# Kernel optimization log

Measured on AMD Instinct MI355X. Metric: run time of the kernel, lower is better.

The kernel has to match this reference:

```python
import jax, jax.numpy as jnp
import numpy as np

B, H, W, C = 16, 256, 256, 32
FILTER = 64


def conv_relu(x, k, b):
    y = jax.lax.conv_general_dilated(x, k, (1, 1), 'VALID',
                                     dimension_numbers=('NHWC', 'HWIO', 'NHWC'))
    return jax.nn.relu(y + b)


def maxpool2(x):
    return jax.lax.reduce_window(x, -jnp.inf, jax.lax.max,
                                 (1, 2, 2, 1), (1, 2, 2, 1), 'VALID')


def affine_grid_generator(theta):
    # tf.meshgrid default 'xy': shapes [W, H]
    xs = jnp.linspace(-1.0, 1.0, H)
    ys = jnp.linspace(-1.0, 1.0, W)
    xT, yT = jnp.meshgrid(xs, ys)
    grid = jnp.stack([xT.ravel(), yT.ravel(), jnp.ones(W * H, jnp.float32)])  # [3, W*H]
    batch_grid = jnp.einsum('bij,jk->bik', theta, grid)  # [B,2,W*H]
    return batch_grid.reshape(B, 2, H, W)


def get_pixel_value(fm, xi, yi):
    b = jnp.arange(B)[:, None, None]
    return fm[b, yi, xi]  # [B,H,W,C]


def bilinear_sampler(fm, x, y):
    max_x = H - 1
    max_y = W - 1
    x = 0.5 * ((x + 1.0) * jnp.float32(max_x - 1))
    y = 0.5 * ((y + 1.0) * jnp.float32(max_y - 1))
    x0 = jnp.floor(x).astype(jnp.int32)
    x1 = x0 + 1
    y0 = jnp.floor(y).astype(jnp.int32)
    y1 = y0 + 1
    x0 = jnp.clip(x0, 0, max_x)
    x1 = jnp.clip(x1, 0, max_x)
    y0 = jnp.clip(y0, 0, max_y)
    y1 = jnp.clip(y1, 0, max_y)
    Ia = get_pixel_value(fm, x0, y0)
    Ib = get_pixel_value(fm, x0, y1)
    Ic = get_pixel_value(fm, x1, y0)
    Id = get_pixel_value(fm, x1, y1)
    x0f, x1f = x0.astype(jnp.float32), x1.astype(jnp.float32)
    y0f, y1f = y0.astype(jnp.float32), y1.astype(jnp.float32)
    wa = ((x1f - x) * (y1f - y))[..., None]
    wb = ((x1f - x) * (y - y0f))[..., None]
    wc = ((x - x0f) * (y1f - y))[..., None]
    wd = ((x - x0f) * (y - y0f))[..., None]
    return wa * Ia + wb * Ib + wc * Ic + wd * Id


def setup_inputs() -> dict:
    key = jax.random.key(0)
    ks = jax.random.split(key, 12)

    def he(k, shape, fan_in):
        return jax.random.normal(k, shape, jnp.float32) * np.sqrt(2.0 / fan_in)

    f4, f2 = FILTER // 4, FILTER // 2
    x = jax.random.normal(ks[0], (B, H, W, C), jnp.float32)
    W1 = he(ks[1], (3, 3, C, f4), 9 * C); b1 = jnp.zeros((f4,), jnp.float32)
    W2 = he(ks[2], (3, 3, f4, f2), 9 * f4); b2 = jnp.zeros((f2,), jnp.float32)
    W3 = he(ks[3], (3, 3, f2, f2), 9 * f2); b3 = jnp.zeros((f2,), jnp.float32)
    D1 = he(ks[4], (f2, FILTER), f2); db1 = jnp.zeros((FILTER,), jnp.float32)
    D2 = he(ks[5], (FILTER, f2), FILTER); db2 = jnp.zeros((f2,), jnp.float32)
    # original inits kernel to zeros, bias to identity transform; use small
    # random kernel so the sampled grid is a non-trivial near-identity warp.
    D3 = jax.random.normal(ks[6], (f2, 6), jnp.float32) * 0.01
    db3 = jnp.array([1.0, 0.0, 0.0, 0.0, 1.0, 0.0], jnp.float32)
    return {"x": x, "W1": W1, "b1": b1, "W2": W2, "b2": b2, "W3": W3, "b3": b3,
            "D1": D1, "db1": db1, "D2": D2, "db2": db2, "D3": D3, "db3": db3}


def reference(x, W1, b1, W2, b2, W3, b3, D1, db1, D2, db2, D3, db3):
    # localization net
    h = maxpool2(conv_relu(x, W1, b1))
    h = maxpool2(conv_relu(h, W2, b2))
    h = maxpool2(conv_relu(h, W3, b3))
    h = jnp.mean(h, axis=(1, 2))  # GlobalAveragePooling2D -> [B, filter//2]
    h = jax.nn.relu(h @ D1 + db1)
    h = jax.nn.relu(h @ D2 + db2)
    theta = (h @ D3 + db3).reshape(B, 2, 3)
    grid = affine_grid_generator(theta)
    xS = grid[:, 0]
    yS = grid[:, 1]
    return bilinear_sampler(x, xS, yS)
```

## Files before the change

### kernel.cpp

```cpp
#include <hip/hip_runtime.h>
#include <hip/hip_bf16.h>


#define P1_ELEMS 4129024
#define P2_ELEMS 1968128
#define P3_ELEMS 460800

#define C1_PXSTR 36
#define C1_ROWSTR (34*36)

__global__ __launch_bounds__(256) void conv1_pool_kernel(
    const float* __restrict__ x, const float* __restrict__ W1,
    const float* __restrict__ b1, float* __restrict__ p1)
{
    __shared__ float xt[10 * C1_ROWSTR];

    const int tid = threadIdx.x;
    const int b   = blockIdx.z;
    const int ph0 = blockIdx.y * 4;
    const int pw0 = blockIdx.x * 16;
    const float* xb = x + (size_t)b * (256*256*32);

    for (int i = tid; i < 10*34*8; i += 256) {
        const int dr  = i / 272;
        const int rem = i - dr * 272;
        const int j   = rem >> 3;
        const int ch  = rem & 7;
        int r_in = 2*ph0 + dr; if (r_in > 255) r_in = 255;
        int c_in = 2*pw0 + j;  if (c_in > 255) c_in = 255;
        const float4 v = *(const float4*)(xb + ((size_t)r_in*256 + c_in)*32 + ch*4);
        *(float4*)(&xt[dr*C1_ROWSTR + j*C1_PXSTR + ch*4]) = v;
    }
    __syncthreads();

    const int fq   = __builtin_amdgcn_readfirstlane(tid >> 6);
    const int lane = tid & 63;
    const int row  = lane >> 4;
    const int col  = lane & 15;

    float4 a0, a1, a2, a3;
    {
        const float4 bv = *(const float4*)(b1 + 4*fq);
        a0 = bv; a1 = bv; a2 = bv; a3 = bv;
    }

    const float* xbase = &xt[(2*row)*C1_ROWSTR + (2*col)*C1_PXSTR];
    const float* wbase = W1 + 4*fq;

#define C1_FMA(A, XV) \
    A.x += XV.x*w0.x; A.y += XV.x*w0.y; A.z += XV.x*w0.z; A.w += XV.x*w0.w; \
    A.x += XV.y*w1.x; A.y += XV.y*w1.y; A.z += XV.y*w1.z; A.w += XV.y*w1.w; \
    A.x += XV.z*w2.x; A.y += XV.z*w2.y; A.z += XV.z*w2.z; A.w += XV.z*w2.w; \
    A.x += XV.w*w3.x; A.y += XV.w*w3.y; A.z += XV.w*w3.z; A.w += XV.w*w3.w;

    #pragma unroll 1
    for (int kh = 0; kh < 3; ++kh) {
      #pragma unroll 1
      for (int kw = 0; kw < 3; ++kw) {
        const float* xp_ = xbase + kh*C1_ROWSTR + kw*C1_PXSTR;
        const float* wp_ = wbase + (kh*3 + kw)*32*16;
        #pragma unroll
        for (int c4 = 0; c4 < 8; ++c4) {
            const float4 x0 = *(const float4*)(xp_ + 4*c4);
            const float4 x1 = *(const float4*)(xp_ + C1_PXSTR + 4*c4);
            const float4 x2 = *(const float4*)(xp_ + C1_ROWSTR + 4*c4);
            const float4 x3 = *(const float4*)(xp_ + C1_ROWSTR + C1_PXSTR + 4*c4);
            const float4 w0 = *(const float4*)(wp_ + (4*c4+0)*16);
            const float4 w1 = *(const float4*)(wp_ + (4*c4+1)*16);
            const float4 w2 = *(const float4*)(wp_ + (4*c4+2)*16);
            const float4 w3 = *(const float4*)(wp_ + (4*c4+3)*16);
            C1_FMA(a0, x0)
            C1_FMA(a1, x1)
            C1_FMA(a2, x2)
            C1_FMA(a3, x3)
        }
      }
    }

    const int ph = ph0 + row, pw = pw0 + col;
    if (ph < 127 && pw < 127) {
        float4 o;
        o.x = fmaxf(fmaxf(fmaxf(a0.x, a1.x), fmaxf(a2.x, a3.x)), 0.0f);
        o.y = fmaxf(fmaxf(fmaxf(a0.y, a1.y), fmaxf(a2.y, a3.y)), 0.0f);
        o.z = fmaxf(fmaxf(fmaxf(a0.z, a1.z), fmaxf(a2.z, a3.z)), 0.0f);
        o.w = fmaxf(fmaxf(fmaxf(a0.w, a1.w), fmaxf(a2.w, a3.w)), 0.0f);
        *(float4*)(p1 + (((size_t)b*127 + ph)*127 + pw) * 16 + 4*fq) = o;
    }
}

#define C2_PXSTR 20
#define C2_ROWSTR (34*20)

__global__ __launch_bounds__(256) void conv2_pool_kernel(
    const float* __restrict__ p1, const float* __restrict__ W2,
    const float* __restrict__ b2, float* __restrict__ p2)
{
    __shared__ float xt[10 * C2_ROWSTR];

    const int tid = threadIdx.x;
    const int b   = blockIdx.z;
    const int ph0 = blockIdx.y * 4;
    const int pw0 = blockIdx.x * 16;
    const float* xb = p1 + (size_t)b * (127*127*16);

    for (int i = tid; i < 10*34*4; i += 256) {
        const int dr  = i / 136;
        const int rem = i - dr * 136;
        const int j   = rem >> 2;
        const int ch  = rem & 3;
        int r_in = 2*ph0 + dr; if (r_in > 126) r_in = 126;
        int c_in = 2*pw0 + j;  if (c_in > 126) c_in = 126;
        const float4 v = *(const float4*)(xb + ((size_t)r_in*127 + c_in)*16 + ch*4);
        *(float4*)(&xt[dr*C2_ROWSTR + j*C2_PXSTR + ch*4]) = v;
    }
    __syncthreads();

    const int wv   = __builtin_amdgcn_readfirstlane(tid >> 6);
    const int lane = tid & 63;
    const int row  = lane >> 4;
    const int col  = lane & 15;
    const int f0   = 8 * wv;

    float4 aA0, aA1, aA2, aA3;
    float4 aB0, aB1, aB2, aB3;
    {
        const float4 bvA = *(const float4*)(b2 + f0);
        const float4 bvB = *(const float4*)(b2 + f0 + 4);
        aA0 = bvA; aA1 = bvA; aA2 = bvA; aA3 = bvA;
        aB0 = bvB; aB1 = bvB; aB2 = bvB; aB3 = bvB;
    }

    const float* xbase = &xt[(2*row)*C2_ROWSTR + (2*col)*C2_PXSTR];
    const float* wbase = W2 + f0;

#define C2_FMA(AA, AB, XC, WA, WB) \
    AA.x += XC*WA.x; AA.y += XC*WA.y; AA.z += XC*WA.z; AA.w += XC*WA.w; \
    AB.x += XC*WB.x; AB.y += XC*WB.y; AB.z += XC*WB.z; AB.w += XC*WB.w;

    #pragma unroll 1
    for (int kh = 0; kh < 3; ++kh) {
      #pragma unroll 1
      for (int kw = 0; kw < 3; ++kw) {
        const float* xp_ = xbase + kh*C2_ROWSTR + kw*C2_PXSTR;
        const float* wp_ = wbase + (kh*3 + kw)*16*32;
        #pragma unroll
        for (int c4 = 0; c4 < 4; ++c4) {
            const float4 x0 = *(const float4*)(xp_ + 4*c4);
            const float4 x1 = *(const float4*)(xp_ + C2_PXSTR + 4*c4);
            const float4 x2 = *(const float4*)(xp_ + C2_ROWSTR + 4*c4);
            const float4 x3 = *(const float4*)(xp_ + C2_ROWSTR + C2_PXSTR + 4*c4);
            #pragma unroll
            for (int c = 0; c < 4; ++c) {
                const float4 wA = *(const float4*)(wp_ + (4*c4+c)*32);
                const float4 wB = *(const float4*)(wp_ + (4*c4+c)*32 + 4);
                const float xc0 = (c==0)?x0.x:(c==1)?x0.y:(c==2)?x0.z:x0.w;
                const float xc1 = (c==0)?x1.x:(c==1)?x1.y:(c==2)?x1.z:x1.w;
                const float xc2 = (c==0)?x2.x:(c==1)?x2.y:(c==2)?x2.z:x2.w;
                const float xc3 = (c==0)?x3.x:(c==1)?x3.y:(c==2)?x3.z:x3.w;
                C2_FMA(aA0, aB0, xc0, wA, wB)
                C2_FMA(aA1, aB1, xc1, wA, wB)
                C2_FMA(aA2, aB2, xc2, wA, wB)
                C2_FMA(aA3, aB3, xc3, wA, wB)
            }
        }
      }
    }

    const int ph = ph0 + row, pw = pw0 + col;
    if (ph < 62 && pw < 62) {
        float4 oA, oB;
        oA.x = fmaxf(fmaxf(fmaxf(aA0.x, aA1.x), fmaxf(aA2.x, aA3.x)), 0.0f);
        oA.y = fmaxf(fmaxf(fmaxf(aA0.y, aA1.y), fmaxf(aA2.y, aA3.y)), 0.0f);
        oA.z = fmaxf(fmaxf(fmaxf(aA0.z, aA1.z), fmaxf(aA2.z, aA3.z)), 0.0f);
        oA.w = fmaxf(fmaxf(fmaxf(aA0.w, aA1.w), fmaxf(aA2.w, aA3.w)), 0.0f);
        oB.x = fmaxf(fmaxf(fmaxf(aB0.x, aB1.x), fmaxf(aB2.x, aB3.x)), 0.0f);
        oB.y = fmaxf(fmaxf(fmaxf(aB0.y, aB1.y), fmaxf(aB2.y, aB3.y)), 0.0f);
        oB.z = fmaxf(fmaxf(fmaxf(aB0.z, aB1.z), fmaxf(aB2.z, aB3.z)), 0.0f);
        oB.w = fmaxf(fmaxf(fmaxf(aB0.w, aB1.w), fmaxf(aB2.w, aB3.w)), 0.0f);
        float* dst = p2 + (((size_t)b*62 + ph)*62 + pw) * 32 + f0;
        *(float4*)(dst)     = oA;
        *(float4*)(dst + 4) = oB;
    }
}

__global__ __launch_bounds__(256) void conv3_pool_kernel(
    const float* __restrict__ p2, const float* __restrict__ W3,
    const float* __restrict__ b3, float* __restrict__ p3)
{
    __shared__ float xt[10 * C1_ROWSTR];

    const int tid = threadIdx.x;
    const int b   = blockIdx.z;
    const int ph0 = blockIdx.y * 4;
    const int pw0 = blockIdx.x * 16;
    const float* xb = p2 + (size_t)b * (62*62*32);

    for (int i = tid; i < 10*34*8; i += 256) {
        const int dr  = i / 272;
        const int rem = i - dr * 272;
        const int j   = rem >> 3;
        const int ch  = rem & 7;
        int r_in = 2*ph0 + dr; if (r_in > 61) r_in = 61;
        int c_in = 2*pw0 + j;  if (c_in > 61) c_in = 61;
        const float4 v = *(const float4*)(xb + ((size_t)r_in*62 + c_in)*32 + ch*4);
        *(float4*)(&xt[dr*C1_ROWSTR + j*C1_PXSTR + ch*4]) = v;
    }
    __syncthreads();

    const int wv   = __builtin_amdgcn_readfirstlane(tid >> 6);
    const int lane = tid & 63;
    const int row  = lane >> 4;
    const int col  = lane & 15;
    const int f0   = 8 * wv;

    float4 aA0, aA1, aA2, aA3;
    float4 aB0, aB1, aB2, aB3;
    {
        const float4 bvA = *(const float4*)(b3 + f0);
        const float4 bvB = *(const float4*)(b3 + f0 + 4);
        aA0 = bvA; aA1 = bvA; aA2 = bvA; aA3 = bvA;
        aB0 = bvB; aB1 = bvB; aB2 = bvB; aB3 = bvB;
    }

    const float* xbase = &xt[(2*row)*C1_ROWSTR + (2*col)*C1_PXSTR];
    const float* wbase = W3 + f0;

    #pragma unroll 1
    for (int kh = 0; kh < 3; ++kh) {
      #pragma unroll 1
      for (int kw = 0; kw < 3; ++kw) {
        const float* xp_ = xbase + kh*C1_ROWSTR + kw*C1_PXSTR;
        const float* wp_ = wbase + (kh*3 + kw)*32*32;
        #pragma unroll
        for (int c4 = 0; c4 < 8; ++c4) {
            const float4 x0 = *(const float4*)(xp_ + 4*c4);
            const float4 x1 = *(const float4*)(xp_ + C1_PXSTR + 4*c4);
            const float4 x2 = *(const float4*)(xp_ + C1_ROWSTR + 4*c4);
            const float4 x3 = *(const float4*)(xp_ + C1_ROWSTR + C1_PXSTR + 4*c4);
            #pragma unroll
            for (int c = 0; c < 4; ++c) {
                const float4 wA = *(const float4*)(wp_ + (4*c4+c)*32);
                const float4 wB = *(const float4*)(wp_ + (4*c4+c)*32 + 4);
                const float xc0 = (c==0)?x0.x:(c==1)?x0.y:(c==2)?x0.z:x0.w;
                const float xc1 = (c==0)?x1.x:(c==1)?x1.y:(c==2)?x1.z:x1.w;
                const float xc2 = (c==0)?x2.x:(c==1)?x2.y:(c==2)?x2.z:x2.w;
                const float xc3 = (c==0)?x3.x:(c==1)?x3.y:(c==2)?x3.z:x3.w;
                C2_FMA(aA0, aB0, xc0, wA, wB)
                C2_FMA(aA1, aB1, xc1, wA, wB)
                C2_FMA(aA2, aB2, xc2, wA, wB)
                C2_FMA(aA3, aB3, xc3, wA, wB)
            }
        }
      }
    }

    const int ph = ph0 + row, pw = pw0 + col;
    if (ph < 30 && pw < 30) {
        float4 oA, oB;
        oA.x = fmaxf(fmaxf(fmaxf(aA0.x, aA1.x), fmaxf(aA2.x, aA3.x)), 0.0f);
        oA.y = fmaxf(fmaxf(fmaxf(aA0.y, aA1.y), fmaxf(aA2.y, aA3.y)), 0.0f);
        oA.z = fmaxf(fmaxf(fmaxf(aA0.z, aA1.z), fmaxf(aA2.z, aA3.z)), 0.0f);
        oA.w = fmaxf(fmaxf(fmaxf(aA0.w, aA1.w), fmaxf(aA2.w, aA3.w)), 0.0f);
        oB.x = fmaxf(fmaxf(fmaxf(aB0.x, aB1.x), fmaxf(aB2.x, aB3.x)), 0.0f);
        oB.y = fmaxf(fmaxf(fmaxf(aB0.y, aB1.y), fmaxf(aB2.y, aB3.y)), 0.0f);
        oB.z = fmaxf(fmaxf(fmaxf(aB0.z, aB1.z), fmaxf(aB2.z, aB3.z)), 0.0f);
        oB.w = fmaxf(fmaxf(fmaxf(aB0.w, aB1.w), fmaxf(aB2.w, aB3.w)), 0.0f);
        float* dst = p3 + (((size_t)b*30 + ph)*30 + pw) * 32 + f0;
        *(float4*)(dst)     = oA;
        *(float4*)(dst + 4) = oB;
    }
}

__global__ __launch_bounds__(256) void head_kernel(
    const float* __restrict__ p3,
    const float* __restrict__ D1, const float* __restrict__ db1,
    const float* __restrict__ D2, const float* __restrict__ db2,
    const float* __restrict__ D3, const float* __restrict__ db3,
    float* __restrict__ theta)
{
    __shared__ float red[8][32];
    __shared__ float hmean[32];
    __shared__ float h1[64];
    __shared__ float h2[32];

    const int b   = blockIdx.x;
    const int tid = threadIdx.x;
    const int c = tid & 31, r = tid >> 5;

    const float* p = p3 + (size_t)b * (900*32);
    float s = 0.0f;
    for (int i = r; i < 900; i += 8) s += p[i*32 + c];
    red[r][c] = s;
    __syncthreads();

    if (tid < 32) {
        float m = 0.0f;
        #pragma unroll
        for (int j = 0; j < 8; ++j) m += red[j][tid];
        hmean[tid] = m * (1.0f / 900.0f);
    }
    __syncthreads();

    if (tid < 64) {
        float a = db1[tid];
        #pragma unroll
        for (int k = 0; k < 32; ++k) a += hmean[k] * D1[k*64 + tid];
        h1[tid] = fmaxf(a, 0.0f);
    }
    __syncthreads();

    if (tid < 32) {
        float a = db2[tid];
        #pragma unroll
        for (int k = 0; k < 64; ++k) a += h1[k] * D2[k*32 + tid];
        h2[tid] = fmaxf(a, 0.0f);
    }
    __syncthreads();

    if (tid < 6) {
        float a = db3[tid];
        #pragma unroll
        for (int k = 0; k < 32; ++k) a += h2[k] * D3[k*6 + tid];
        theta[b*6 + tid] = a;
    }
}

__global__ __launch_bounds__(256) void sampler_kernel(
    const float* __restrict__ x, const float* __restrict__ theta,
    float* __restrict__ out)
{
    const int t  = blockIdx.x * 256 + threadIdx.x;
    const int c4 = t & 7;
    const int w  = (t >> 3) & 255;
    const int h  = (t >> 11) & 255;
    const int b  = t >> 19;

    const float* th = theta + b*6;
    const float gx = -1.0f + (float)w * (2.0f / 255.0f);
    const float gy = -1.0f + (float)h * (2.0f / 255.0f);
    const float xS = th[0]*gx + th[1]*gy + th[2];
    const float yS = th[3]*gx + th[4]*gy + th[5];
    const float xp = 0.5f * (xS + 1.0f) * 254.0f;
    const float yp = 0.5f * (yS + 1.0f) * 254.0f;

    int x0 = (int)floorf(xp), y0 = (int)floorf(yp);
    int x1 = x0 + 1,          y1 = y0 + 1;
    x0 = x0 < 0 ? 0 : (x0 > 255 ? 255 : x0);
    x1 = x1 < 0 ? 0 : (x1 > 255 ? 255 : x1);
    y0 = y0 < 0 ? 0 : (y0 > 255 ? 255 : y0);
    y1 = y1 < 0 ? 0 : (y1 > 255 ? 255 : y1);

    const float x0f = (float)x0, x1f = (float)x1;
    const float y0f = (float)y0, y1f = (float)y1;
    const float wa = (x1f - xp) * (y1f - yp);
    const float wb = (x1f - xp) * (yp - y0f);
    const float wc = (xp - x0f) * (y1f - yp);
    const float wd = (xp - x0f) * (yp - y0f);

    const float* xb = x + (size_t)b * (256*256*32) + c4*4;
    const float4 Ia = *(const float4*)(xb + ((size_t)y0*256 + x0)*32);
    const float4 Ib = *(const float4*)(xb + ((size_t)y1*256 + x0)*32);
    const float4 Ic = *(const float4*)(xb + ((size_t)y0*256 + x1)*32);
    const float4 Id = *(const float4*)(xb + ((size_t)y1*256 + x1)*32);

    float4 o;
    o.x = wa*Ia.x + wb*Ib.x + wc*Ic.x + wd*Id.x;
    o.y = wa*Ia.y + wb*Ib.y + wc*Ic.y + wd*Id.y;
    o.z = wa*Ia.z + wb*Ib.z + wc*Ic.z + wd*Id.z;
    o.w = wa*Ia.w + wb*Ib.w + wc*Ic.w + wd*Id.w;
    ((float4*)out)[t] = o;
}

extern "C" void kernel_launch(void* const* d_in, const int* in_sizes, int n_in,
                              void* d_out, int out_size, void* d_ws, size_t ws_size,
                              hipStream_t stream) {
    const float* x   = (const float*)d_in[0];
    const float* W1  = (const float*)d_in[1];
    const float* b1  = (const float*)d_in[2];
    const float* W2  = (const float*)d_in[3];
    const float* b2  = (const float*)d_in[4];
    const float* W3  = (const float*)d_in[5];
    const float* b3  = (const float*)d_in[6];
    const float* D1  = (const float*)d_in[7];
    const float* db1 = (const float*)d_in[8];
    const float* D2  = (const float*)d_in[9];
    const float* db2 = (const float*)d_in[10];
    const float* D3  = (const float*)d_in[11];
    const float* db3 = (const float*)d_in[12];
    float* out = (float*)d_out;

    float* p1    = (float*)d_ws;
    float* p2    = p1 + P1_ELEMS;
    float* p3    = p2 + P2_ELEMS;
    float* theta = p3 + P3_ELEMS;

    conv1_pool_kernel<<<dim3(8, 32, 16), 256, 0, stream>>>(x,  W1, b1, p1);
    conv2_pool_kernel<<<dim3(4, 16, 16), 256, 0, stream>>>(p1, W2, b2, p2);
    conv3_pool_kernel<<<dim3(2, 8, 16),  256, 0, stream>>>(p2, W3, b3, p3);
    head_kernel      <<<dim3(16),        256, 0, stream>>>(p3, D1, db1, D2, db2, D3, db3, theta);
    sampler_kernel   <<<dim3(32768),     256, 0, stream>>>(x, theta, out);
}
```

Baseline: 485.1 us.

## Unify conv-pool kernels with channel-planar LDS and per-thread full filter outputs

Replaces the three hand-written conv+ReLU+maxpool kernels with one templated kernel. The LDS tile now uses a channel-plane float4 layout, and each thread computes one conv output pixel across all filters instead of four pool-window pixels over a filter slice. The 2x2 max-pool is done with cross-lane shuffles. This removes the duplicated per-filter-group work and changes how LDS is accessed, but it raises per-thread accumulator registers (32 floats) and leaves only a quarter of the lanes doing the stores.

```diff
diff --git a/kernel.cpp b/kernel.cpp
--- a/kernel.cpp
+++ b/kernel.cpp
@@ -6,268 +6,89 @@
 #define P2_ELEMS 1968128
 #define P3_ELEMS 460800
 
-#define C1_PXSTR 36
-#define C1_ROWSTR (34*36)
-
-__global__ __launch_bounds__(256) void conv1_pool_kernel(
-    const float* __restrict__ x, const float* __restrict__ W1,
-    const float* __restrict__ b1, float* __restrict__ p1)
+
+template<int CH, int F, int IN_HW, int POOL_HW>
+__global__ __launch_bounds__(256) void conv_pool_kernel(
+    const float* __restrict__ in, const float* __restrict__ Wt,
+    const float* __restrict__ bias, float* __restrict__ out)
 {
-    __shared__ float xt[10 * C1_ROWSTR];
+    constexpr int PLANES = CH / 4;
+    constexpr int LP     = (PLANES == 8) ? 3 : 2;
+    constexpr int PSTR   = 341;
+    __shared__ float4 xt[PLANES * PSTR];
 
     const int tid = threadIdx.x;
     const int b   = blockIdx.z;
-    const int ph0 = blockIdx.y * 4;
-    const int pw0 = blockIdx.x * 16;
-    const float* xb = x + (size_t)b * (256*256*32);
-
-    for (int i = tid; i < 10*34*8; i += 256) {
-        const int dr  = i / 272;
-        const int rem = i - dr * 272;
-        const int j   = rem >> 3;
-        const int ch  = rem & 7;
-        int r_in = 2*ph0 + dr; if (r_in > 255) r_in = 255;
-        int c_in = 2*pw0 + j;  if (c_in > 255) c_in = 255;
-        const float4 v = *(const float4*)(xb + ((size_t)r_in*256 + c_in)*32 + ch*4);
-        *(float4*)(&xt[dr*C1_ROWSTR + j*C1_PXSTR + ch*4]) = v;
-    }
-    __syncthreads();
-
-    const int fq   = __builtin_amdgcn_readfirstlane(tid >> 6);
+    const int r0  = blockIdx.y * 8;
+    const int c0  = blockIdx.x * 32;
+    const float* ib = in + (size_t)b * (IN_HW * IN_HW * CH);
+
+    for (int idx = tid; idx < 340 * PLANES; idx += 256) {
+        const int ch4 = idx & (PLANES - 1);
+        const int pix = idx >> LP;
+        const int dr  = pix / 34;
+        const int j   = pix - dr * 34;
+        int r = r0 + dr; if (r > IN_HW - 1) r = IN_HW - 1;
+        int c = c0 + j;  if (c > IN_HW - 1) c = IN_HW - 1;
+        xt[ch4 * PSTR + pix] =
+            *(const float4*)(ib + ((size_t)r * IN_HW + c) * CH + ch4 * 4);
+    }
+    __syncthreads();
+
+    const int wv   = tid >> 6;
     const int lane = tid & 63;
-    const int row  = lane >> 4;
-    const int col  = lane & 15;
-
-    float4 a0, a1, a2, a3;
-    {
-        const float4 bv = *(const float4*)(b1 + 4*fq);
-        a0 = bv; a1 = bv; a2 = bv; a3 = bv;
-    }
-
-    const float* xbase = &xt[(2*row)*C1_ROWSTR + (2*col)*C1_PXSTR];
-    const float* wbase = W1 + 4*fq;
-
-#define C1_FMA(A, XV) \
-    A.x += XV.x*w0.x; A.y += XV.x*w0.y; A.z += XV.x*w0.z; A.w += XV.x*w0.w; \
-    A.x += XV.y*w1.x; A.y += XV.y*w1.y; A.z += XV.y*w1.z; A.w += XV.y*w1.w; \
-    A.x += XV.z*w2.x; A.y += XV.z*w2.y; A.z += XV.z*w2.z; A.w += XV.z*w2.w; \
-    A.x += XV.w*w3.x; A.y += XV.w*w3.y; A.z += XV.w*w3.z; A.w += XV.w*w3.w;
+    const int ccol = lane & 31;
+    const int px0  = (2 * wv + (lane >> 5)) * 34 + ccol;
+
+    float4 acc[F / 4];
+    #pragma unroll
+    for (int q = 0; q < F / 4; ++q) acc[q] = *(const float4*)(bias + 4 * q);
 
     #pragma unroll 1
     for (int kh = 0; kh < 3; ++kh) {
       #pragma unroll 1
       for (int kw = 0; kw < 3; ++kw) {
-        const float* xp_ = xbase + kh*C1_ROWSTR + kw*C1_PXSTR;
-        const float* wp_ = wbase + (kh*3 + kw)*32*16;
-        #pragma unroll
-        for (int c4 = 0; c4 < 8; ++c4) {
-            const float4 x0 = *(const float4*)(xp_ + 4*c4);
-            const float4 x1 = *(const float4*)(xp_ + C1_PXSTR + 4*c4);
-            const float4 x2 = *(const float4*)(xp_ + C1_ROWSTR + 4*c4);
-            const float4 x3 = *(const float4*)(xp_ + C1_ROWSTR + C1_PXSTR + 4*c4);
-            const float4 w0 = *(const float4*)(wp_ + (4*c4+0)*16);
-            const float4 w1 = *(const float4*)(wp_ + (4*c4+1)*16);
-            const float4 w2 = *(const float4*)(wp_ + (4*c4+2)*16);
-            const float4 w3 = *(const float4*)(wp_ + (4*c4+3)*16);
-            C1_FMA(a0, x0)
-            C1_FMA(a1, x1)
-            C1_FMA(a2, x2)
-            C1_FMA(a3, x3)
-        }
-      }
-    }
-
-    const int ph = ph0 + row, pw = pw0 + col;
-    if (ph < 127 && pw < 127) {
-        float4 o;
-        o.x = fmaxf(fmaxf(fmaxf(a0.x, a1.x), fmaxf(a2.x, a3.x)), 0.0f);
-        o.y = fmaxf(fmaxf(fmaxf(a0.y, a1.y), fmaxf(a2.y, a3.y)), 0.0f);
-        o.z = fmaxf(fmaxf(fmaxf(a0.z, a1.z), fmaxf(a2.z, a3.z)), 0.0f);
-        o.w = fmaxf(fmaxf(fmaxf(a0.w, a1.w), fmaxf(a2.w, a3.w)), 0.0f);
-        *(float4*)(p1 + (((size_t)b*127 + ph)*127 + pw) * 16 + 4*fq) = o;
-    }
-}
-
-#define C2_PXSTR 20
-#define C2_ROWSTR (34*20)
-
-__global__ __launch_bounds__(256) void conv2_pool_kernel(
-    const float* __restrict__ p1, const float* __restrict__ W2,
-    const float* __restrict__ b2, float* __restrict__ p2)
-{
-    __shared__ float xt[10 * C2_ROWSTR];
-
-    const int tid = threadIdx.x;
-    const int b   = blockIdx.z;
-    const int ph0 = blockIdx.y * 4;
-    const int pw0 = blockIdx.x * 16;
-    const float* xb = p1 + (size_t)b * (127*127*16);
-
-    for (int i = tid; i < 10*34*4; i += 256) {
-        const int dr  = i / 136;
-        const int rem = i - dr * 136;
-        const int j   = rem >> 2;
-        const int ch  = rem & 3;
-        int r_in = 2*ph0 + dr; if (r_in > 126) r_in = 126;
-        int c_in = 2*pw0 + j;  if (c_in > 126) c_in = 126;
-        const float4 v = *(const float4*)(xb + ((size_t)r_in*127 + c_in)*16 + ch*4);
-        *(float4*)(&xt[dr*C2_ROWSTR + j*C2_PXSTR + ch*4]) = v;
-    }
-    __syncthreads();
-
-    const int wv   = __builtin_amdgcn_readfirstlane(tid >> 6);
-    const int lane = tid & 63;
-    const int row  = lane >> 4;
-    const int col  = lane & 15;
-    const int f0   = 8 * wv;
-
-    float4 aA0, aA1, aA2, aA3;
-    float4 aB0, aB1, aB2, aB3;
-    {
-        const float4 bvA = *(const float4*)(b2 + f0);
-        const float4 bvB = *(const float4*)(b2 + f0 + 4);
-        aA0 = bvA; aA1 = bvA; aA2 = bvA; aA3 = bvA;
-        aB0 = bvB; aB1 = bvB; aB2 = bvB; aB3 = bvB;
-    }
-
-    const float* xbase = &xt[(2*row)*C2_ROWSTR + (2*col)*C2_PXSTR];
-    const float* wbase = W2 + f0;
-
-#define C2_FMA(AA, AB, XC, WA, WB) \
-    AA.x += XC*WA.x; AA.y += XC*WA.y; AA.z += XC*WA.z; AA.w += XC*WA.w; \
-    AB.x += XC*WB.x; AB.y += XC*WB.y; AB.z += XC*WB.z; AB.w += XC*WB.w;
-
-    #pragma unroll 1
-    for (int kh = 0; kh < 3; ++kh) {
-      #pragma unroll 1
-      for (int kw = 0; kw < 3; ++kw) {
-        const float* xp_ = xbase + kh*C2_ROWSTR + kw*C2_PXSTR;
-        const float* wp_ = wbase + (kh*3 + kw)*16*32;
-        #pragma unroll
-        for (int c4 = 0; c4 < 4; ++c4) {
-            const float4 x0 = *(const float4*)(xp_ + 4*c4);
-            const float4 x1 = *(const float4*)(xp_ + C2_PXSTR + 4*c4);
-            const float4 x2 = *(const float4*)(xp_ + C2_ROWSTR + 4*c4);
-            const float4 x3 = *(const float4*)(xp_ + C2_ROWSTR + C2_PXSTR + 4*c4);
+        const float* wp = Wt + (kh * 3 + kw) * CH * F;
+        const int px = px0 + kh * 34 + kw;
+        #pragma unroll
+        for (int c4 = 0; c4 < PLANES; ++c4) {
+            const float4 xv = xt[c4 * PSTR + px];
             #pragma unroll
-            for (int c = 0; c < 4; ++c) {
-                const float4 wA = *(const float4*)(wp_ + (4*c4+c)*32);
-                const float4 wB = *(const float4*)(wp_ + (4*c4+c)*32 + 4);
-                const float xc0 = (c==0)?x0.x:(c==1)?x0.y:(c==2)?x0.z:x0.w;
-                const float xc1 = (c==0)?x1.x:(c==1)?x1.y:(c==2)?x1.z:x1.w;
-                const float xc2 = (c==0)?x2.x:(c==1)?x2.y:(c==2)?x2.z:x2.w;
-                const float xc3 = (c==0)?x3.x:(c==1)?x3.y:(c==2)?x3.z:x3.w;
-                C2_FMA(aA0, aB0, xc0, wA, wB)
-                C2_FMA(aA1, aB1, xc1, wA, wB)
-                C2_FMA(aA2, aB2, xc2, wA, wB)
-                C2_FMA(aA3, aB3, xc3, wA, wB)
+            for (int cc = 0; cc < 4; ++cc) {
+                const float xc = (cc == 0) ? xv.x : (cc == 1) ? xv.y
+                               : (cc == 2) ? xv.z : xv.w;
+                const float* wr = wp + (4 * c4 + cc) * F;
+                #pragma unroll
+                for (int q = 0; q < F / 4; ++q) {
+                    const float4 w4 = *(const float4*)(wr + 4 * q);
+                    acc[q].x += xc * w4.x; acc[q].y += xc * w4.y;
+                    acc[q].z += xc * w4.z; acc[q].w += xc * w4.w;
+                }
             }
         }
       }
     }
 
-    const int ph = ph0 + row, pw = pw0 + col;
-    if (ph < 62 && pw < 62) {
-        float4 oA, oB;
-        oA.x = fmaxf(fmaxf(fmaxf(aA0.x, aA1.x), fmaxf(aA2.x, aA3.x)), 0.0f);
-        oA.y = fmaxf(fmaxf(fmaxf(aA0.y, aA1.y), fmaxf(aA2.y, aA3.y)), 0.0f);
-        oA.z = fmaxf(fmaxf(fmaxf(aA0.z, aA1.z), fmaxf(aA2.z, aA3.z)), 0.0f);
-        oA.w = fmaxf(fmaxf(fmaxf(aA0.w, aA1.w), fmaxf(aA2.w, aA3.w)), 0.0f);
-        oB.x = fmaxf(fmaxf(fmaxf(aB0.x, aB1.x), fmaxf(aB2.x, aB3.x)), 0.0f);
-        oB.y = fmaxf(fmaxf(fmaxf(aB0.y, aB1.y), fmaxf(aB2.y, aB3.y)), 0.0f);
-        oB.z = fmaxf(fmaxf(fmaxf(aB0.z, aB1.z), fmaxf(aB2.z, aB3.z)), 0.0f);
-        oB.w = fmaxf(fmaxf(fmaxf(aB0.w, aB1.w), fmaxf(aB2.w, aB3.w)), 0.0f);
-        float* dst = p2 + (((size_t)b*62 + ph)*62 + pw) * 32 + f0;
-        *(float4*)(dst)     = oA;
-        *(float4*)(dst + 4) = oB;
-    }
-}
-
-__global__ __launch_bounds__(256) void conv3_pool_kernel(
-    const float* __restrict__ p2, const float* __restrict__ W3,
-    const float* __restrict__ b3, float* __restrict__ p3)
-{
-    __shared__ float xt[10 * C1_ROWSTR];
-
-    const int tid = threadIdx.x;
-    const int b   = blockIdx.z;
-    const int ph0 = blockIdx.y * 4;
-    const int pw0 = blockIdx.x * 16;
-    const float* xb = p2 + (size_t)b * (62*62*32);
-
-    for (int i = tid; i < 10*34*8; i += 256) {
-        const int dr  = i / 272;
-        const int rem = i - dr * 272;
-        const int j   = rem >> 3;
-        const int ch  = rem & 7;
-        int r_in = 2*ph0 + dr; if (r_in > 61) r_in = 61;
-        int c_in = 2*pw0 + j;  if (c_in > 61) c_in = 61;
-        const float4 v = *(const float4*)(xb + ((size_t)r_in*62 + c_in)*32 + ch*4);
-        *(float4*)(&xt[dr*C1_ROWSTR + j*C1_PXSTR + ch*4]) = v;
-    }
-    __syncthreads();
-
-    const int wv   = __builtin_amdgcn_readfirstlane(tid >> 6);
-    const int lane = tid & 63;
-    const int row  = lane >> 4;
-    const int col  = lane & 15;
-    const int f0   = 8 * wv;
-
-    float4 aA0, aA1, aA2, aA3;
-    float4 aB0, aB1, aB2, aB3;
-    {
-        const float4 bvA = *(const float4*)(b3 + f0);
-        const float4 bvB = *(const float4*)(b3 + f0 + 4);
-        aA0 = bvA; aA1 = bvA; aA2 = bvA; aA3 = bvA;
-        aB0 = bvB; aB1 = bvB; aB2 = bvB; aB3 = bvB;
-    }
-
-    const float* xbase = &xt[(2*row)*C1_ROWSTR + (2*col)*C1_PXSTR];
-    const float* wbase = W3 + f0;
-
-    #pragma unroll 1
-    for (int kh = 0; kh < 3; ++kh) {
-      #pragma unroll 1
-      for (int kw = 0; kw < 3; ++kw) {
-        const float* xp_ = xbase + kh*C1_ROWSTR + kw*C1_PXSTR;
-        const float* wp_ = wbase + (kh*3 + kw)*32*32;
-        #pragma unroll
-        for (int c4 = 0; c4 < 8; ++c4) {
-            const float4 x0 = *(const float4*)(xp_ + 4*c4);
-            const float4 x1 = *(const float4*)(xp_ + C1_PXSTR + 4*c4);
-            const float4 x2 = *(const float4*)(xp_ + C1_ROWSTR + 4*c4);
-            const float4 x3 = *(const float4*)(xp_ + C1_ROWSTR + C1_PXSTR + 4*c4);
-            #pragma unroll
-            for (int c = 0; c < 4; ++c) {
-                const float4 wA = *(const float4*)(wp_ + (4*c4+c)*32);
-                const float4 wB = *(const float4*)(wp_ + (4*c4+c)*32 + 4);
-                const float xc0 = (c==0)?x0.x:(c==1)?x0.y:(c==2)?x0.z:x0.w;
-                const float xc1 = (c==0)?x1.x:(c==1)?x1.y:(c==2)?x1.z:x1.w;
-                const float xc2 = (c==0)?x2.x:(c==1)?x2.y:(c==2)?x2.z:x2.w;
-                const float xc3 = (c==0)?x3.x:(c==1)?x3.y:(c==2)?x3.z:x3.w;
-                C2_FMA(aA0, aB0, xc0, wA, wB)
-                C2_FMA(aA1, aB1, xc1, wA, wB)
-                C2_FMA(aA2, aB2, xc2, wA, wB)
-                C2_FMA(aA3, aB3, xc3, wA, wB)
-            }
-        }
-      }
-    }
-
-    const int ph = ph0 + row, pw = pw0 + col;
-    if (ph < 30 && pw < 30) {
-        float4 oA, oB;
-        oA.x = fmaxf(fmaxf(fmaxf(aA0.x, aA1.x), fmaxf(aA2.x, aA3.x)), 0.0f);
-        oA.y = fmaxf(fmaxf(fmaxf(aA0.y, aA1.y), fmaxf(aA2.y, aA3.y)), 0.0f);
-        oA.z = fmaxf(fmaxf(fmaxf(aA0.z, aA1.z), fmaxf(aA2.z, aA3.z)), 0.0f);
-        oA.w = fmaxf(fmaxf(fmaxf(aA0.w, aA1.w), fmaxf(aA2.w, aA3.w)), 0.0f);
-        oB.x = fmaxf(fmaxf(fmaxf(aB0.x, aB1.x), fmaxf(aB2.x, aB3.x)), 0.0f);
-        oB.y = fmaxf(fmaxf(fmaxf(aB0.y, aB1.y), fmaxf(aB2.y, aB3.y)), 0.0f);
-        oB.z = fmaxf(fmaxf(fmaxf(aB0.z, aB1.z), fmaxf(aB2.z, aB3.z)), 0.0f);
-        oB.w = fmaxf(fmaxf(fmaxf(aB0.w, aB1.w), fmaxf(aB2.w, aB3.w)), 0.0f);
-        float* dst = p3 + (((size_t)b*30 + ph)*30 + pw) * 32 + f0;
-        *(float4*)(dst)     = oA;
-        *(float4*)(dst + 4) = oB;
+    #pragma unroll
+    for (int q = 0; q < F / 4; ++q) {
+        float4 v = acc[q];
+        v.x = fmaxf(v.x, __shfl_xor(v.x, 1));
+        v.y = fmaxf(v.y, __shfl_xor(v.y, 1));
+        v.z = fmaxf(v.z, __shfl_xor(v.z, 1));
+        v.w = fmaxf(v.w, __shfl_xor(v.w, 1));
+        v.x = fmaxf(fmaxf(v.x, __shfl_xor(v.x, 32)), 0.0f);
+        v.y = fmaxf(fmaxf(v.y, __shfl_xor(v.y, 32)), 0.0f);
+        v.z = fmaxf(fmaxf(v.z, __shfl_xor(v.z, 32)), 0.0f);
+        v.w = fmaxf(fmaxf(v.w, __shfl_xor(v.w, 32)), 0.0f);
+        acc[q] = v;
+    }
+
+    const int pr = blockIdx.y * 4 + wv;
+    const int pc = blockIdx.x * 16 + (ccol >> 1);
+    if ((lane & 1) == 0 && lane < 32 && pr < POOL_HW && pc < POOL_HW) {
+        float* dst = out + (((size_t)b * POOL_HW + pr) * POOL_HW + pc) * F;
+        #pragma unroll
+        for (int q = 0; q < F / 4; ++q) *(float4*)(dst + 4 * q) = acc[q];
     }
 }
 
@@ -394,9 +215,9 @@
     float* p3    = p2 + P2_ELEMS;
     float* theta = p3 + P3_ELEMS;
 
-    conv1_pool_kernel<<<dim3(8, 32, 16), 256, 0, stream>>>(x,  W1, b1, p1);
-    conv2_pool_kernel<<<dim3(4, 16, 16), 256, 0, stream>>>(p1, W2, b2, p2);
-    conv3_pool_kernel<<<dim3(2, 8, 16),  256, 0, stream>>>(p2, W3, b3, p3);
-    head_kernel      <<<dim3(16),        256, 0, stream>>>(p3, D1, db1, D2, db2, D3, db3, theta);
-    sampler_kernel   <<<dim3(32768),     256, 0, stream>>>(x, theta, out);
-}
+    conv_pool_kernel<32, 16, 256, 127><<<dim3(8, 32, 16), 256, 0, stream>>>(x,  W1, b1, p1);
+    conv_pool_kernel<16, 32, 127,  62><<<dim3(4, 16, 16), 256, 0, stream>>>(p1, W2, b2, p2);
+    conv_pool_kernel<32, 32,  62,  30><<<dim3(2, 8, 16),  256, 0, stream>>>(p2, W3, b3, p3);
+    head_kernel      <<<dim3(16),    256, 0, stream>>>(p3, D1, db1, D2, db2, D3, db3, theta);
+    sampler_kernel   <<<dim3(32768), 256, 0, stream>>>(x, theta, out);
+}
```

Result: no change. 493.4 us (+1.7%).
